# Kernel tuning notes

Hardware: AMD Instinct MI355X
Metric: run time of the kernel (lower is better)

Reference implementation:

```python
import jax, jax.numpy as jnp
import numpy as np

N_HEADS = 32
EPS = 1e-7
ROPE_BASE = 10000.0


def rms_norm(x, gamma):
    return x / jnp.sqrt(EPS + jnp.mean(x * x, axis=-1, keepdims=True)) * gamma


def rope_tables(seq_len, head_dim, dtype=jnp.float32):
    inv_freq = 1.0 / (ROPE_BASE ** (jnp.arange(0, head_dim, 2, dtype=jnp.float32) / head_dim))
    angles = jnp.arange(seq_len, dtype=jnp.float32)[:, None] * inv_freq[None, :]  # [S, D/2]
    angles = jnp.concatenate([angles, angles], axis=-1)  # [S, D]
    return jnp.cos(angles).astype(dtype), jnp.sin(angles).astype(dtype)


def apply_rope(x, cos, sin):
    # x: [B, H, S, D]; cos/sin: [S, D]
    d = x.shape[-1]
    x1, x2 = x[..., : d // 2], x[..., d // 2 :]
    rotated = jnp.concatenate([-x2, x1], axis=-1)
    return x * cos[None, None] + rotated * sin[None, None]


def setup_inputs() -> dict:
    key = jax.random.key(0)
    ks = jax.random.split(key, 9)
    B, S, D, Hd = 1, 2048, 4096, 11008
    s = lambda k, shape, fan: jax.random.normal(k, shape, jnp.float32) * (fan ** -0.5)
    return {
        "X": jax.random.normal(ks[0], (B, S, D), jnp.float32),
        "Wq": s(ks[1], (D, D), D),
        "Wk": s(ks[2], (D, D), D),
        "Wv": s(ks[3], (D, D), D),
        "Wo": s(ks[4], (D, D), D),
        "bo": jnp.zeros((D,), jnp.float32),
        "gamma1": jnp.ones((D,), jnp.float32),
        "gamma2": jnp.ones((D,), jnp.float32),
        "W1": s(ks[5], (D, Hd), D),
        "W2": s(ks[6], (D, Hd), D),
        "W3": s(ks[7], (Hd, D), Hd),
    }


def reference(X, Wq, Wk, Wv, Wo, bo, gamma1, gamma2, W1, W2, W3):
    B, S, D = X.shape
    H = N_HEADS
    hd = D // H

    # --- attention sublayer ---
    h = rms_norm(X, gamma1)
    q = (h @ Wq).reshape(B, S, H, hd).transpose(0, 2, 1, 3)  # [B,H,S,hd]
    k = (h @ Wk).reshape(B, S, H, hd).transpose(0, 2, 1, 3)
    v = (h @ Wv).reshape(B, S, H, hd).transpose(0, 2, 1, 3)

    cos, sin = rope_tables(S, hd, X.dtype)
    q = apply_rope(q, cos, sin)
    k = apply_rope(k, cos, sin)

    scores = jnp.einsum("bhsd,bhtd->bhst", q, k) / jnp.sqrt(jnp.asarray(hd, X.dtype))
    causal = jnp.tril(jnp.ones((S, S), bool))
    scores = jnp.where(causal, scores, -jnp.inf)
    attn = jax.nn.softmax(scores, axis=-1)
    out = jnp.einsum("bhst,bhtd->bhsd", attn, v)
    out = out.transpose(0, 2, 1, 3).reshape(B, S, D)
    out = out @ Wo + bo
    X = X + out

    # --- SwiGLU FFN sublayer ---
    h2 = rms_norm(X, gamma2)
    x1 = h2 @ W1
    x2 = h2 @ W2
    ff = (x1 * jax.nn.sigmoid(x1) * x2) @ W3
    return X + ff
```

## Files before the change

kernel.cpp:

```cpp
#include <hip/hip_runtime.h>
#include <hip/hip_bf16.h>
#include <cstdint>
#include <cmath>

typedef __bf16 bf16;
typedef __attribute__((ext_vector_type(8))) __bf16 bf16x8;
typedef __attribute__((ext_vector_type(4))) __bf16 bf16x4;
typedef __attribute__((ext_vector_type(4))) float f32x4;

__device__ __forceinline__ void gload_lds16(const void* g, void* l) {
  __builtin_amdgcn_global_load_lds((__attribute__((address_space(1))) void*)g,
                                   (__attribute__((address_space(3))) void*)l,
                                   16, 0, 0);
}

template<int BM, int EPI>
__global__ __launch_bounds__(512, 2) void gemmd(
    const bf16* __restrict__ A, const bf16* __restrict__ Bt, void* __restrict__ Cv,
    const float* __restrict__ bias, const float* __restrict__ resid,
    const float* __restrict__ cosT, const float* __restrict__ sinT,
    bf16* __restrict__ q_out, bf16* __restrict__ k_out, bf16* __restrict__ v_out,
    int M, int N, int K, int gm) {
  extern __shared__ char lds[];
  constexpr int ASZ = BM * 128;
  constexpr int BUFS = ASZ + 32768;
  constexpr int MF = BM / 64;
  constexpr int LA = BM / 64;

  const int tid = threadIdx.x;
  const int wave = tid >> 6, lane = tid & 63;
  const int wr = wave >> 1, wc = wave & 1;
  const int l15 = lane & 15, l4 = lane >> 4;
  const int qq = gridDim.x >> 3;
  const int wgid = (blockIdx.x & 7) * qq + (blockIdx.x >> 3);
  const int tm = wgid % gm, tn = wgid / gm;
  const long brow = (long)tm * BM, bcol = (long)tn * 256;
  const int NT = K >> 6;
  const bf16* Ab = A + brow * K;
  const bf16* Bb = Bt + bcol * K;

  f32x4 acc[MF][8];
  #pragma unroll
  for (int i = 0; i < MF; ++i)
    #pragma unroll
    for (int j = 0; j < 8; ++j) acc[i][j] = (f32x4){0.f, 0.f, 0.f, 0.f};

  bf16x8 a[MF][2], b[8][2];

  auto stage = [&](int T) {
    const long kofs = (long)T << 6;
    char* wb = lds + (T & 1) * BUFS;
    #pragma unroll
    for (int i = 0; i < LA; ++i) {
      const int slot = i * 512 + tid, r = slot >> 3, c0 = slot & 7;
      gload_lds16(Ab + (long)r * K + kofs + ((c0 ^ (r & 7)) << 3), wb + slot * 16);
    }
    #pragma unroll
    for (int i = 0; i < 4; ++i) {
      const int slot = i * 512 + tid, r = slot >> 3, c0 = slot & 7;
      gload_lds16(Bb + (long)r * K + kofs + ((c0 ^ (r & 7)) << 3), wb + ASZ + slot * 16);
    }
  };

  stage(0);
  __syncthreads();

  for (int g = 0; g < NT; ++g) {
    const int pg = (g & 1) * BUFS;
    if (g + 1 < NT) stage(g + 1);
    #pragma unroll
    for (int nf = 0; nf < 8; ++nf)
      #pragma unroll
      for (int ks = 0; ks < 2; ++ks) {
        const int r = wc * 128 + nf * 16 + l15;
        b[nf][ks] = *(const bf16x8*)(lds + pg + ASZ + r * 128 + (((ks * 4 + l4) ^ (r & 7)) << 4));
      }
    #pragma unroll
    for (int mf = 0; mf < MF; ++mf)
      #pragma unroll
      for (int ks = 0; ks < 2; ++ks) {
        const int r = wr * (BM / 4) + mf * 16 + l15;
        a[mf][ks] = *(const bf16x8*)(lds + pg + r * 128 + (((ks * 4 + l4) ^ (r & 7)) << 4));
      }
    #pragma unroll
    for (int ks = 0; ks < 2; ++ks)
      #pragma unroll
      for (int mf = 0; mf < MF; ++mf)
        #pragma unroll
        for (int nf = 0; nf < 8; ++nf)
          acc[mf][nf] = __builtin_amdgcn_mfma_f32_16x16x32_bf16(
              a[mf][ks], b[nf][ks], acc[mf][nf], 0, 0, 0);
    __syncthreads();
  }

  if (EPI == 1 || EPI == 2) {
    #pragma unroll
    for (int mf = 0; mf < MF; ++mf) {
      const long row0 = brow + wr * (BM / 4) + mf * 16 + l4 * 4;
      #pragma unroll
      for (int nf = 0; nf < 8; ++nf) {
        const long col = bcol + wc * 128 + nf * 16 + l15;
        #pragma unroll
        for (int rj = 0; rj < 4; ++rj) {
          const long idx = (row0 + rj) * N + col;
          const float v = acc[mf][nf][rj];
          if (EPI == 1) ((float*)Cv)[idx] = v + bias[col] + resid[idx];
          else          ((float*)Cv)[idx] = v + resid[idx];
        }
      }
    }
  } else if (EPI == 3) {
    const int region = (int)(bcol >> 12);
    const int hc = (int)(bcol & 4095) + wc * 128;
    const int h = hc >> 7;
    if (region < 2) {
      bf16* dh = (region == 0 ? q_out : k_out) + (long)h * 2048 * 128;
      #pragma unroll
      for (int mf = 0; mf < MF; ++mf) {
        #pragma unroll
        for (int rj = 0; rj < 4; ++rj) {
          const int s = (int)brow + wr * (BM / 4) + mf * 16 + l4 * 4 + rj;
          const float* cr = cosT + s * 64;
          const float* sr = sinT + s * 64;
          #pragma unroll
          for (int nfp = 0; nfp < 4; ++nfp) {
            const int d = nfp * 16 + l15;
            const float c = cr[d], sn = sr[d];
            const float x1 = acc[mf][nfp][rj], x2 = acc[mf][nfp + 4][rj];
            dh[(long)s * 128 + d]      = (bf16)(x1 * c - x2 * sn);
            dh[(long)s * 128 + d + 64] = (bf16)(x2 * c + x1 * sn);
          }
        }
      }
    } else {
      bf16* dh = v_out + (long)h * 128 * 2048;
      #pragma unroll
      for (int mf = 0; mf < MF; ++mf) {
        const int s0 = (int)brow + wr * (BM / 4) + mf * 16 + l4 * 4;
        #pragma unroll
        for (int nf = 0; nf < 8; ++nf) {
          const int d = nf * 16 + l15;
          bf16x4 v;
          #pragma unroll
          for (int rj = 0; rj < 4; ++rj) v[rj] = (bf16)acc[mf][nf][rj];
          *(bf16x4*)(dh + (long)d * 2048 + s0) = v;
        }
      }
    }
  } else {
    #pragma unroll
    for (int mf = 0; mf < MF; ++mf) {
      #pragma unroll
      for (int rj = 0; rj < 4; ++rj) {
        const int s = (int)brow + wr * (BM / 4) + mf * 16 + l4 * 4 + rj;
        bf16* gr = (bf16*)Cv + (long)s * 11008;
        #pragma unroll
        for (int nfp = 0; nfp < 4; ++nfp) {
          const int col = (int)bcol + wc * 128 + nfp * 32 + l15;
          const int j = ((col >> 5) << 4) + l15;
          const float x1 = acc[mf][2 * nfp][rj], x2 = acc[mf][2 * nfp + 1][rj];
          const float sg = x1 / (1.f + __expf(-x1));
          gr[j] = (bf16)(sg * x2);
        }
      }
    }
  }
}

__global__ __launch_bounds__(256) void rmsnorm_kernel(
    const float* __restrict__ X, const float* __restrict__ gamma,
    bf16* __restrict__ out, int D) {
  const int row = blockIdx.x;
  const float* xr = X + (long)row * D;
  float ss = 0.f;
  for (int i = threadIdx.x * 4; i < D; i += 1024) {
    float4 v = *(const float4*)(xr + i);
    ss += v.x * v.x + v.y * v.y + v.z * v.z + v.w * v.w;
  }
  #pragma unroll
  for (int off = 32; off; off >>= 1) ss += __shfl_down(ss, off, 64);
  __shared__ float wsum[4];
  if ((threadIdx.x & 63) == 0) wsum[threadIdx.x >> 6] = ss;
  __syncthreads();
  const float tot = wsum[0] + wsum[1] + wsum[2] + wsum[3];
  const float scale = rsqrtf(1e-7f + tot / (float)D);
  bf16* orow = out + (long)row * D;
  for (int i = threadIdx.x * 4; i < D; i += 1024) {
    float4 v = *(const float4*)(xr + i);
    float4 g = *(const float4*)(gamma + i);
    orow[i]     = (bf16)(v.x * scale * g.x);
    orow[i + 1] = (bf16)(v.y * scale * g.y);
    orow[i + 2] = (bf16)(v.z * scale * g.z);
    orow[i + 3] = (bf16)(v.w * scale * g.w);
  }
}

__global__ __launch_bounds__(256) void wtrans_kernel(
    const float* __restrict__ in, bf16* __restrict__ out, int R, int C) {
  __shared__ float t[64][65];
  const int bx = blockIdx.x, by = blockIdx.y;
  const int tx = threadIdx.x & 63, ty = threadIdx.x >> 6;
  #pragma unroll
  for (int i = 0; i < 64; i += 4)
    t[ty + i][tx] = in[(long)(by * 64 + ty + i) * C + bx * 64 + tx];
  __syncthreads();
  #pragma unroll
  for (int i = 0; i < 64; i += 4)
    out[(long)(bx * 64 + ty + i) * R + by * 64 + tx] = (bf16)t[tx][ty + i];
}

__global__ __launch_bounds__(256) void w12trans_kernel(
    const float* __restrict__ in, bf16* __restrict__ out, int off) {
  __shared__ float t[32][33];
  const int bx = blockIdx.x, by = blockIdx.y;
  const int tx = threadIdx.x & 31, ty = threadIdx.x >> 5;
  #pragma unroll
  for (int i = 0; i < 32; i += 8)
    t[ty + i][tx] = in[(long)(by * 32 + ty + i) * 11008 + bx * 32 + tx];
  __syncthreads();
  #pragma unroll
  for (int i = 0; i < 32; i += 8) {
    const int j = bx * 32 + ty + i;
    const int r = ((j >> 4) << 5) + off + (j & 15);
    out[(long)r * 4096 + by * 32 + tx] = (bf16)t[tx][ty + i];
  }
}

__global__ __launch_bounds__(256) void rope_table_kernel(float* __restrict__ cosT,
                                                         float* __restrict__ sinT) {
  const int idx = blockIdx.x * 256 + threadIdx.x;
  const int i = idx & 63, s = idx >> 6;
  const float inv = powf(10000.f, -(float)i / 64.f);
  const float ang = (float)s * inv;
  cosT[idx] = cosf(ang);
  sinT[idx] = sinf(ang);
}

__global__ __launch_bounds__(256) void attn_kernel(
    const bf16* __restrict__ qh, const bf16* __restrict__ kh,
    const bf16* __restrict__ vt, bf16* __restrict__ outb) {
  constexpr int S = 2048;
  const int qb = blockIdx.x, head = blockIdx.y;
  const int tid = threadIdx.x, wave = tid >> 6, lane = tid & 63;
  __shared__ bf16 Ks[64 * 128];
  __shared__ bf16 Vs[128 * 64];
  __shared__ bf16 Plds[4][16 * 64];
  const bf16* qhh = qh + (long)head * S * 128;
  const bf16* khh = kh + (long)head * S * 128;
  const bf16* vth = vt + (long)head * 128 * S;

  const int l15 = lane & 15, l4 = lane >> 4;
  const int qrow = qb * 64 + wave * 16 + l15;
  bf16x8 qf[4];
  #pragma unroll
  for (int kf = 0; kf < 4; ++kf)
    qf[kf] = *(const bf16x8*)(qhh + (long)qrow * 128 + kf * 32 + l4 * 8);

  float m_r[4], l_r[4];
  #pragma unroll
  for (int r = 0; r < 4; ++r) { m_r[r] = -INFINITY; l_r[r] = 0.f; }
  f32x4 oacc[8] = {};
  const float scale = 0.08838834764831845f;

  for (int tb = 0; tb <= qb; ++tb) {
    #pragma unroll
    for (int i = 0; i < 4; ++i) {
      const int c = wave + 4 * i;
      gload_lds16(khh + (long)(tb * 64 + c * 4 + l4) * 128 + l15 * 8, Ks + c * 512);
      gload_lds16(vth + (long)(c * 8 + (lane >> 3)) * S + tb * 64 + (lane & 7) * 8, Vs + c * 512);
    }
    __syncthreads();

    f32x4 sf[4];
    #pragma unroll
    for (int ft = 0; ft < 4; ++ft) {
      f32x4 acn = {};
      #pragma unroll
      for (int kf = 0; kf < 4; ++kf) {
        bf16x8 kfr = *(const bf16x8*)(Ks + (ft * 16 + l15) * 128 + kf * 32 + l4 * 8);
        acn = __builtin_amdgcn_mfma_f32_16x16x32_bf16(qf[kf], kfr, acn, 0, 0, 0);
      }
      #pragma unroll
      for (int r = 0; r < 4; ++r) sf[ft][r] = acn[r] * scale;
    }
    if (tb == qb) {
      #pragma unroll
      for (int ft = 0; ft < 4; ++ft) {
        const int t_l = ft * 16 + l15;
        #pragma unroll
        for (int r = 0; r < 4; ++r)
          if (t_l > wave * 16 + l4 * 4 + r) sf[ft][r] = -INFINITY;
      }
    }
    float scl[4];
    #pragma unroll
    for (int r = 0; r < 4; ++r) {
      float mx = fmaxf(fmaxf(sf[0][r], sf[1][r]), fmaxf(sf[2][r], sf[3][r]));
      mx = fmaxf(mx, __shfl_xor(mx, 1, 64));
      mx = fmaxf(mx, __shfl_xor(mx, 2, 64));
      mx = fmaxf(mx, __shfl_xor(mx, 4, 64));
      mx = fmaxf(mx, __shfl_xor(mx, 8, 64));
      const float mnew = fmaxf(m_r[r], mx);
      scl[r] = __expf(m_r[r] - mnew);
      m_r[r] = mnew;
      float rs = 0.f;
      #pragma unroll
      for (int ft = 0; ft < 4; ++ft) {
        const float pexp = __expf(sf[ft][r] - mnew);
        sf[ft][r] = pexp;
        rs += pexp;
      }
      rs += __shfl_xor(rs, 1, 64);
      rs += __shfl_xor(rs, 2, 64);
      rs += __shfl_xor(rs, 4, 64);
      rs += __shfl_xor(rs, 8, 64);
      l_r[r] = l_r[r] * scl[r] + rs;
    }
    #pragma unroll
    for (int ft = 0; ft < 4; ++ft)
      #pragma unroll
      for (int r = 0; r < 4; ++r)
        Plds[wave][(l4 * 4 + r) * 64 + ft * 16 + l15] = (bf16)sf[ft][r];
    #pragma unroll
    for (int fd = 0; fd < 8; ++fd)
      #pragma unroll
      for (int r = 0; r < 4; ++r) oacc[fd][r] *= scl[r];
    #pragma unroll
    for (int fd = 0; fd < 8; ++fd) {
      #pragma unroll
      for (int kt = 0; kt < 2; ++kt) {
        bf16x8 pa = *(const bf16x8*)(&Plds[wave][l15 * 64 + kt * 32 + l4 * 8]);
        bf16x8 vb = *(const bf16x8*)(Vs + (fd * 16 + l15) * 64 + kt * 32 + l4 * 8);
        oacc[fd] = __builtin_amdgcn_mfma_f32_16x16x32_bf16(pa, vb, oacc[fd], 0, 0, 0);
      }
    }
    __syncthreads();
  }
  #pragma unroll
  for (int fd = 0; fd < 8; ++fd) {
    #pragma unroll
    for (int r = 0; r < 4; ++r) {
      const long row = qb * 64 + wave * 16 + l4 * 4 + r;
      outb[row * 4096 + head * 128 + fd * 16 + l15] = (bf16)(oacc[fd][r] / l_r[r]);
    }
  }
}

extern "C" void kernel_launch(void* const* d_in, const int* in_sizes, int n_in,
                              void* d_out, int out_size, void* d_ws, size_t ws_size,
                              hipStream_t stream) {
  const float* X  = (const float*)d_in[0];
  const float* Wq = (const float*)d_in[1];
  const float* Wk = (const float*)d_in[2];
  const float* Wv = (const float*)d_in[3];
  const float* Wo = (const float*)d_in[4];
  const float* bo = (const float*)d_in[5];
  const float* g1 = (const float*)d_in[6];
  const float* g2 = (const float*)d_in[7];
  const float* W1 = (const float*)d_in[8];
  const float* W2 = (const float*)d_in[9];
  const float* W3 = (const float*)d_in[10];
  float* out = (float*)d_out;

  hipFuncSetAttribute((const void*)gemmd<256, 3>, hipFuncAttributeMaxDynamicSharedMemorySize, 131072);
  hipFuncSetAttribute((const void*)gemmd<256, 4>, hipFuncAttributeMaxDynamicSharedMemorySize, 131072);
  hipFuncSetAttribute((const void*)gemmd<128, 1>, hipFuncAttributeMaxDynamicSharedMemorySize, 98304);
  hipFuncSetAttribute((const void*)gemmd<128, 2>, hipFuncAttributeMaxDynamicSharedMemorySize, 98304);

  char* p = (char*)d_ws;
  auto alloc = [&](size_t bytes) {
    char* r = p;
    p += (bytes + 255) & ~(size_t)255;
    return r;
  };
  float* cosT = (float*)alloc(2048 * 64 * 4);
  float* sinT = (float*)alloc(2048 * 64 * 4);
  bf16* WqkvT = (bf16*)alloc(12288L * 4096 * 2);
  bf16* WoT  = (bf16*)alloc(4096L * 4096 * 2);
  bf16* W12T = (bf16*)alloc(22016L * 4096 * 2);
  bf16* W3T  = (bf16*)alloc(4096L * 11008 * 2);
  bf16* qhB  = (bf16*)alloc(2048L * 4096 * 2);
  bf16* khB  = (bf16*)alloc(2048L * 4096 * 2);
  bf16* vtB  = (bf16*)alloc(2048L * 4096 * 2);
  bf16* hbuf = (bf16*)alloc(2048L * 4096 * 2);
  bf16* h2   = (bf16*)alloc(2048L * 4096 * 2);
  float* X2  = (float*)alloc(2048L * 4096 * 4);

  bf16* gsw = (bf16*)WqkvT;
  bf16* attnb = hbuf;

  rope_table_kernel<<<512, 256, 0, stream>>>(cosT, sinT);
  wtrans_kernel<<<dim3(64, 64), 256, 0, stream>>>(Wq, WqkvT, 4096, 4096);
  wtrans_kernel<<<dim3(64, 64), 256, 0, stream>>>(Wk, WqkvT + 4096L * 4096, 4096, 4096);
  wtrans_kernel<<<dim3(64, 64), 256, 0, stream>>>(Wv, WqkvT + 2 * 4096L * 4096, 4096, 4096);
  wtrans_kernel<<<dim3(64, 64), 256, 0, stream>>>(Wo, WoT, 4096, 4096);
  w12trans_kernel<<<dim3(344, 128), 256, 0, stream>>>(W1, W12T, 0);
  w12trans_kernel<<<dim3(344, 128), 256, 0, stream>>>(W2, W12T, 16);
  wtrans_kernel<<<dim3(64, 172), 256, 0, stream>>>(W3, W3T, 11008, 4096);

  rmsnorm_kernel<<<2048, 256, 0, stream>>>(X, g1, hbuf, 4096);

  gemmd<256, 3><<<384, 512, 131072, stream>>>(hbuf, WqkvT, nullptr, nullptr, nullptr,
                                              cosT, sinT, qhB, khB, vtB,
                                              2048, 12288, 4096, 8);

  attn_kernel<<<dim3(32, 32), 256, 0, stream>>>(qhB, khB, vtB, attnb);

  gemmd<128, 1><<<256, 512, 98304, stream>>>(attnb, WoT, X2, bo, X,
                                             nullptr, nullptr, nullptr, nullptr, nullptr,
                                             2048, 4096, 4096, 16);

  rmsnorm_kernel<<<2048, 256, 0, stream>>>(X2, g2, h2, 4096);

  gemmd<256, 4><<<688, 512, 131072, stream>>>(h2, W12T, gsw, nullptr, nullptr,
                                              nullptr, nullptr, nullptr, nullptr, nullptr,
                                              2048, 22016, 4096, 8);

  gemmd<128, 2><<<256, 512, 98304, stream>>>(gsw, W3T, out, nullptr, X2,
                                             nullptr, nullptr, nullptr, nullptr, nullptr,
                                             2048, 4096, 11008, 16);
}
```

Measured before the change: 1.449 ms.

## Vectorize weight transpose kernels and raise wave priority around MFMA loop

The weight transpose kernels now read float4 and write bf16x4, using 64x64 tiles throughout. The goal is wider, more coalesced global accesses in the per-call fp32-to-bf16 weight conversion. The GEMM main loop also wraps its MFMA block in s_setprio(1)/s_setprio(0) so the matrix-issuing wave is favoured over waves issuing loads. The new LDS read pattern in the transpose strides by 65 floats across rows, which may cause some bank conflicts.

```diff
diff --git a/kernel.cpp b/kernel.cpp
--- a/kernel.cpp
+++ b/kernel.cpp
@@ -82,6 +82,7 @@
         const int r = wr * (BM / 4) + mf * 16 + l15;
         a[mf][ks] = *(const bf16x8*)(lds + pg + r * 128 + (((ks * 4 + l4) ^ (r & 7)) << 4));
       }
+    __builtin_amdgcn_s_setprio(1);
     #pragma unroll
     for (int ks = 0; ks < 2; ++ks)
       #pragma unroll
@@ -90,6 +91,7 @@
         for (int nf = 0; nf < 8; ++nf)
           acc[mf][nf] = __builtin_amdgcn_mfma_f32_16x16x32_bf16(
               a[mf][ks], b[nf][ks], acc[mf][nf], 0, 0, 0);
+    __builtin_amdgcn_s_setprio(0);
     __syncthreads();
   }
 
@@ -199,30 +201,50 @@
     const float* __restrict__ in, bf16* __restrict__ out, int R, int C) {
   __shared__ float t[64][65];
   const int bx = blockIdx.x, by = blockIdx.y;
-  const int tx = threadIdx.x & 63, ty = threadIdx.x >> 6;
-  #pragma unroll
-  for (int i = 0; i < 64; i += 4)
-    t[ty + i][tx] = in[(long)(by * 64 + ty + i) * C + bx * 64 + tx];
+  const int lr = threadIdx.x >> 4;
+  const int lc4 = (threadIdx.x & 15) * 4;
+  #pragma unroll
+  for (int i = 0; i < 4; ++i) {
+    const int r = lr + i * 16;
+    const float4 v = *(const float4*)(in + (long)(by * 64 + r) * C + bx * 64 + lc4);
+    t[r][lc4] = v.x; t[r][lc4 + 1] = v.y; t[r][lc4 + 2] = v.z; t[r][lc4 + 3] = v.w;
+  }
   __syncthreads();
-  #pragma unroll
-  for (int i = 0; i < 64; i += 4)
-    out[(long)(bx * 64 + ty + i) * R + by * 64 + tx] = (bf16)t[tx][ty + i];
+  const int oc = threadIdx.x >> 4;
+  const int or4 = (threadIdx.x & 15) * 4;
+  #pragma unroll
+  for (int i = 0; i < 4; ++i) {
+    const int c = oc + i * 16;
+    bf16x4 v;
+    #pragma unroll
+    for (int j = 0; j < 4; ++j) v[j] = (bf16)t[or4 + j][c];
+    *(bf16x4*)(out + (long)(bx * 64 + c) * R + by * 64 + or4) = v;
+  }
 }
 
 __global__ __launch_bounds__(256) void w12trans_kernel(
     const float* __restrict__ in, bf16* __restrict__ out, int off) {
-  __shared__ float t[32][33];
+  __shared__ float t[64][65];
   const int bx = blockIdx.x, by = blockIdx.y;
-  const int tx = threadIdx.x & 31, ty = threadIdx.x >> 5;
-  #pragma unroll
-  for (int i = 0; i < 32; i += 8)
-    t[ty + i][tx] = in[(long)(by * 32 + ty + i) * 11008 + bx * 32 + tx];
+  const int lk = threadIdx.x >> 4;
+  const int lj4 = (threadIdx.x & 15) * 4;
+  #pragma unroll
+  for (int i = 0; i < 4; ++i) {
+    const int k = lk + i * 16;
+    const float4 v = *(const float4*)(in + (long)(by * 64 + k) * 11008 + bx * 64 + lj4);
+    t[k][lj4] = v.x; t[k][lj4 + 1] = v.y; t[k][lj4 + 2] = v.z; t[k][lj4 + 3] = v.w;
+  }
   __syncthreads();
-  #pragma unroll
-  for (int i = 0; i < 32; i += 8) {
-    const int j = bx * 32 + ty + i;
+  const int oj = threadIdx.x >> 4;
+  const int ok4 = (threadIdx.x & 15) * 4;
+  #pragma unroll
+  for (int i = 0; i < 4; ++i) {
+    const int j = bx * 64 + oj + i * 16;
     const int r = ((j >> 4) << 5) + off + (j & 15);
-    out[(long)r * 4096 + by * 32 + tx] = (bf16)t[tx][ty + i];
+    bf16x4 v;
+    #pragma unroll
+    for (int jj = 0; jj < 4; ++jj) v[jj] = (bf16)t[ok4 + jj][oj + i * 16];
+    *(bf16x4*)(out + (long)r * 4096 + by * 64 + ok4) = v;
   }
 }
 
@@ -394,8 +416,8 @@
   wtrans_kernel<<<dim3(64, 64), 256, 0, stream>>>(Wk, WqkvT + 4096L * 4096, 4096, 4096);
   wtrans_kernel<<<dim3(64, 64), 256, 0, stream>>>(Wv, WqkvT + 2 * 4096L * 4096, 4096, 4096);
   wtrans_kernel<<<dim3(64, 64), 256, 0, stream>>>(Wo, WoT, 4096, 4096);
-  w12trans_kernel<<<dim3(344, 128), 256, 0, stream>>>(W1, W12T, 0);
-  w12trans_kernel<<<dim3(344, 128), 256, 0, stream>>>(W2, W12T, 16);
+  w12trans_kernel<<<dim3(172, 64), 256, 0, stream>>>(W1, W12T, 0);
+  w12trans_kernel<<<dim3(172, 64), 256, 0, stream>>>(W2, W12T, 16);
   wtrans_kernel<<<dim3(64, 172), 256, 0, stream>>>(W3, W3T, 11008, 4096);
 
   rmsnorm_kernel<<<2048, 256, 0, stream>>>(X, g1, hbuf, 4096);
```

Result: faster. 1.373 ms (-5.3%).
